# Kernel tuning notes

Hardware: AMD Instinct MI355X
Metric: run time of the kernel (lower is better)

## Reference

```python
import jax, jax.numpy as jnp
import numpy as np

NEG_SLOPE = 0.2
LN_EPS = 1e-5


def _gat_layer(x, src, dst, W, a_src, a_dst, N):
    # x: [N, Fin], W: [Fin, H*C], a_src/a_dst: [H, C]
    H, C = a_src.shape
    h = (x @ W).reshape(N, H, C)
    al_src = (h * a_src).sum(-1)  # [N, H]
    al_dst = (h * a_dst).sum(-1)  # [N, H]
    e = jax.nn.leaky_relu(al_src[src] + al_dst[dst], NEG_SLOPE)  # [E, H]
    m = jax.ops.segment_max(e, dst, num_segments=N)
    e = jnp.exp(e - m[dst])
    denom = jax.ops.segment_sum(e, dst, num_segments=N)
    alpha = e / denom[dst]  # softmax over incoming edges per dst node
    msg = h[src] * alpha[:, :, None]  # [E, H, C]
    return jax.ops.segment_sum(msg, dst, num_segments=N)  # [N, H, C]


def _layer_norm(x, g, b):
    mu = x.mean(-1, keepdims=True)
    var = ((x - mu) ** 2).mean(-1, keepdims=True)
    return (x - mu) * jax.lax.rsqrt(var + LN_EPS) * g + b


def setup_inputs() -> dict:
    key = jax.random.key(0)
    ks = jax.random.split(key, 20)
    N, E, Fin, Ch, H = 50000, 800000, 128, 64, 4
    s = lambda k, shp, sc=0.05: jax.random.normal(k, shp, dtype=jnp.float32) * sc
    return {
        "x": jax.random.normal(ks[0], (N, Fin), dtype=jnp.float32),
        "edge_index": jax.random.randint(ks[1], (2, E), 0, N, dtype=jnp.int64),
        "W1": s(ks[2], (Fin, H * Ch)),
        "att_src1": s(ks[3], (H, Ch)),
        "att_dst1": s(ks[4], (H, Ch)),
        "b1": jnp.zeros((H * Ch,), jnp.float32),
        "ln1_g": jnp.ones((H * Ch,), jnp.float32),
        "ln1_b": jnp.zeros((H * Ch,), jnp.float32),
        "W2": s(ks[5], (H * Ch, Ch)),
        "att_src2": s(ks[6], (1, Ch)),
        "att_dst2": s(ks[7], (1, Ch)),
        "b2": jnp.zeros((Ch,), jnp.float32),
        "ln2_g": jnp.ones((Ch,), jnp.float32),
        "ln2_b": jnp.zeros((Ch,), jnp.float32),
        "fc1_W": s(ks[8], (Ch, Ch // 2)),
        "fc1_b": jnp.zeros((Ch // 2,), jnp.float32),
        "fc2_W": s(ks[9], (Ch // 2, 1)),
        "fc2_b": jnp.zeros((1,), jnp.float32),
    }


def reference(x, edge_index, W1, att_src1, att_dst1, b1, ln1_g, ln1_b,
              W2, att_src2, att_dst2, b2, ln2_g, ln2_b,
              fc1_W, fc1_b, fc2_W, fc2_b):
    N = x.shape[0]
    # PyG GATConv adds self-loops by default
    loop = jnp.arange(N, dtype=edge_index.dtype)
    src = jnp.concatenate([edge_index[0], loop])
    dst = jnp.concatenate([edge_index[1], loop])

    # GAT layer 1 (heads=4, concat) + LayerNorm + ReLU (dropout is identity in eval)
    h = _gat_layer(x, src, dst, W1, att_src1, att_dst1, N).reshape(N, -1) + b1
    h = jax.nn.relu(_layer_norm(h, ln1_g, ln1_b))

    # GAT layer 2 (heads=1) + LayerNorm + ReLU
    h = _gat_layer(h, src, dst, W2, att_src2, att_dst2, N).reshape(N, -1) + b2
    h = jax.nn.relu(_layer_norm(h, ln2_g, ln2_b))

    # MLP head
    h = jax.nn.relu(h @ fc1_W + fc1_b)
    return h @ fc2_W + fc2_b  # [N, 1]
```

## Files before the change

kernel.cpp:

```cpp
#include <hip/hip_runtime.h>
#include <hip/hip_fp16.h>
#include <math.h>

#define NEG_SLOPE 0.2f
#define LN_EPS 1e-5f
#define SCCHUNK 8192
#define PADCAP 64
#define CURPAD 32

typedef __attribute__((ext_vector_type(8))) _Float16 half8;
typedef __attribute__((ext_vector_type(4))) _Float16 half4;
typedef __attribute__((ext_vector_type(4))) float floatx4;

static __device__ __forceinline__ float lrelu(float e) {
    return e > 0.0f ? e : NEG_SLOPE * e;
}

__global__ __launch_bounds__(256) void k_g1sc(
    const float* __restrict__ x, const float* __restrict__ W1,
    const float* __restrict__ as1, const float* __restrict__ ad1,
    _Float16* __restrict__ h1, float* __restrict__ als, float* __restrict__ ald,
    const int* __restrict__ ei, unsigned* __restrict__ cursor,
    unsigned short* __restrict__ eidx,
    int N, int E, int nsc)
{
    const int tid = threadIdx.x;

    if ((int)blockIdx.x < nsc) {
        const unsigned basev = cursor[(size_t)N * CURPAD];
        const int Et = E + N;
        const int i0 = blockIdx.x * SCCHUNK;
#pragma unroll 4
        for (int j = 0; j < SCCHUNK / 256; ++j) {
            int i = i0 + j * 256 + tid;
            if (i < Et) {
                int s, d;
                if (i < E) { s = ei[i]; d = ei[E + i]; } else { s = d = i - E; }
                unsigned pos = atomicAdd(&cursor[(size_t)d * CURPAD], 1u) - basev;
                if (pos < PADCAP) eidx[(size_t)d * PADCAP + pos] = (unsigned short)s;
            }
        }
        return;
    }

    const int tile = blockIdx.x - nsc;
    const int lane = tid & 63, w = tid >> 6;
    const int l15 = lane & 15, quad = lane >> 4;
    const int r_base = tile * 64;

    half8 B[4][4];
    float asv[4], adv[4];
#pragma unroll
    for (int nt = 0; nt < 4; ++nt) {
        const int n = w * 64 + nt * 16 + l15;
        asv[nt] = as1[n]; adv[nt] = ad1[n];
#pragma unroll
        for (int ks = 0; ks < 4; ++ks) {
            const int k0 = ks * 32 + quad * 8;
            half8 b;
#pragma unroll
            for (int j = 0; j < 8; ++j) b[j] = (_Float16)W1[(size_t)(k0 + j) * 256 + n];
            B[ks][nt] = b;
        }
    }

#pragma unroll
    for (int rt = 0; rt < 4; ++rt) {
        const int r0 = r_base + rt * 16;
        int m = r0 + l15; if (m >= N) m = N - 1;
        half8 A[4];
#pragma unroll
        for (int ks = 0; ks < 4; ++ks) {
            const int k0 = ks * 32 + quad * 8;
            const float4* xp = (const float4*)(x + (size_t)m * 128 + k0);
            float4 v0 = xp[0], v1 = xp[1];
            half8 a;
            a[0] = (_Float16)v0.x; a[1] = (_Float16)v0.y; a[2] = (_Float16)v0.z; a[3] = (_Float16)v0.w;
            a[4] = (_Float16)v1.x; a[5] = (_Float16)v1.y; a[6] = (_Float16)v1.z; a[7] = (_Float16)v1.w;
            A[ks] = a;
        }
        floatx4 C[4];
#pragma unroll
        for (int nt = 0; nt < 4; ++nt) C[nt] = (floatx4){0.f, 0.f, 0.f, 0.f};
#pragma unroll
        for (int ks = 0; ks < 4; ++ks)
#pragma unroll
            for (int nt = 0; nt < 4; ++nt)
                C[nt] = __builtin_amdgcn_mfma_f32_16x16x32_f16(A[ks], B[ks][nt], C[nt], 0, 0, 0);

#pragma unroll
        for (int reg = 0; reg < 4; ++reg) {
            const int row = r0 + quad * 4 + reg;
            float vs = 0.f, vd = 0.f;
#pragma unroll
            for (int nt = 0; nt < 4; ++nt) {
                float c = C[nt][reg];
                if (row < N) h1[(size_t)row * 256 + w * 64 + nt * 16 + l15] = (_Float16)c;
                vs += c * asv[nt]; vd += c * adv[nt];
            }
#pragma unroll
            for (int o = 1; o < 16; o <<= 1) { vs += __shfl_xor(vs, o); vd += __shfl_xor(vd, o); }
            if (l15 == 0 && row < N) { als[row * 4 + w] = vs; ald[row * 4 + w] = vd; }
        }
    }
}

__global__ __launch_bounds__(256) void k_agg1(
    const _Float16* __restrict__ h1, const float* __restrict__ als, const float* __restrict__ ald,
    const unsigned* __restrict__ cursor, const unsigned short* __restrict__ eidx,
    const float* __restrict__ b1, const float* __restrict__ g1, const float* __restrict__ be1,
    _Float16* __restrict__ hln1, int N)
{
    __shared__ float alp[4][64][4];
    __shared__ int   srcl[4][64];
    const int wv = threadIdx.x >> 6, lane = threadIdx.x & 63;
    int n = blockIdx.x * 4 + wv;
    if (n >= N) n = N - 1;
    const int base = n * PADCAP;
    const unsigned basev = cursor[(size_t)N * CURPAD];
    int deg = (int)(cursor[(size_t)n * CURPAD] - basev); if (deg > PADCAP) deg = PADCAP;
    const float4 ad = ((const float4*)ald)[n];

    const int srcv = eidx[base + (lane < deg ? lane : deg - 1)];
    float e0 = -1e30f, e1 = -1e30f, e2 = -1e30f, e3 = -1e30f;
    if (lane < deg) {
        float4 a4 = ((const float4*)als)[srcv];
        e0 = lrelu(a4.x + ad.x);
        e1 = lrelu(a4.y + ad.y);
        e2 = lrelu(a4.z + ad.z);
        e3 = lrelu(a4.w + ad.w);
    }
    float m0 = e0, m1 = e1, m2 = e2, m3 = e3;
#pragma unroll
    for (int o = 32; o; o >>= 1) {
        m0 = fmaxf(m0, __shfl_xor(m0, o));
        m1 = fmaxf(m1, __shfl_xor(m1, o));
        m2 = fmaxf(m2, __shfl_xor(m2, o));
        m3 = fmaxf(m3, __shfl_xor(m3, o));
    }
    float p0 = __expf(e0 - m0), p1 = __expf(e1 - m1);
    float p2 = __expf(e2 - m2), p3 = __expf(e3 - m3);
    float s0 = p0, s1 = p1, s2 = p2, s3 = p3;
#pragma unroll
    for (int o = 32; o; o >>= 1) {
        s0 += __shfl_xor(s0, o);
        s1 += __shfl_xor(s1, o);
        s2 += __shfl_xor(s2, o);
        s3 += __shfl_xor(s3, o);
    }
    float4 av;
    av.x = p0 / s0; av.y = p1 / s1; av.z = p2 / s2; av.w = p3 / s3;
    *(float4*)(&alp[wv][lane][0]) = av;
    srcl[wv][lane] = srcv;

    const int half_ = lane >> 5, l31 = lane & 31, hd = l31 >> 3;
    float4 a0 = make_float4(0.f, 0.f, 0.f, 0.f);
    float4 a1 = make_float4(0.f, 0.f, 0.f, 0.f);
    const int degr = (deg + 7) & ~7;
    for (int eb = 0; eb < degr; eb += 8) {
#pragma unroll
        for (int u = 0; u < 4; ++u) {
            const int e = eb + 2 * u + half_;
            int s = srcl[wv][e];
            float ae = alp[wv][e][hd];
            half8 v = *(const half8*)(h1 + (size_t)s * 256 + l31 * 8);
            a0.x = fmaf((float)v[0], ae, a0.x);
            a0.y = fmaf((float)v[1], ae, a0.y);
            a0.z = fmaf((float)v[2], ae, a0.z);
            a0.w = fmaf((float)v[3], ae, a0.w);
            a1.x = fmaf((float)v[4], ae, a1.x);
            a1.y = fmaf((float)v[5], ae, a1.y);
            a1.z = fmaf((float)v[6], ae, a1.z);
            a1.w = fmaf((float)v[7], ae, a1.w);
        }
    }
    a0.x += __shfl_xor(a0.x, 32); a0.y += __shfl_xor(a0.y, 32);
    a0.z += __shfl_xor(a0.z, 32); a0.w += __shfl_xor(a0.w, 32);
    a1.x += __shfl_xor(a1.x, 32); a1.y += __shfl_xor(a1.y, 32);
    a1.z += __shfl_xor(a1.z, 32); a1.w += __shfl_xor(a1.w, 32);

    const float4 bb0 = ((const float4*)b1)[l31 * 2];
    const float4 bb1 = ((const float4*)b1)[l31 * 2 + 1];
    float y0 = a0.x + bb0.x, y1 = a0.y + bb0.y, y2 = a0.z + bb0.z, y3 = a0.w + bb0.w;
    float y4 = a1.x + bb1.x, y5 = a1.y + bb1.y, y6 = a1.z + bb1.z, y7 = a1.w + bb1.w;
    float ps  = y0 + y1 + y2 + y3 + y4 + y5 + y6 + y7;
    float pss = y0*y0 + y1*y1 + y2*y2 + y3*y3 + y4*y4 + y5*y5 + y6*y6 + y7*y7;
#pragma unroll
    for (int o = 32; o; o >>= 1) { ps += __shfl_xor(ps, o); pss += __shfl_xor(pss, o); }
    float mu = ps * (1.f / 512.f);
    float var = pss * (1.f / 512.f) - mu * mu;
    float rstd = rsqrtf(var + LN_EPS);
    const float4 gg0 = ((const float4*)g1)[l31 * 2];
    const float4 gg1 = ((const float4*)g1)[l31 * 2 + 1];
    const float4 be0 = ((const float4*)be1)[l31 * 2];
    const float4 be1v = ((const float4*)be1)[l31 * 2 + 1];
    if (lane < 32) {
        half8 outv;
        outv[0] = (_Float16)fmaxf((y0 - mu) * rstd * gg0.x + be0.x, 0.f);
        outv[1] = (_Float16)fmaxf((y1 - mu) * rstd * gg0.y + be0.y, 0.f);
        outv[2] = (_Float16)fmaxf((y2 - mu) * rstd * gg0.z + be0.z, 0.f);
        outv[3] = (_Float16)fmaxf((y3 - mu) * rstd * gg0.w + be0.w, 0.f);
        outv[4] = (_Float16)fmaxf((y4 - mu) * rstd * gg1.x + be1v.x, 0.f);
        outv[5] = (_Float16)fmaxf((y5 - mu) * rstd * gg1.y + be1v.y, 0.f);
        outv[6] = (_Float16)fmaxf((y6 - mu) * rstd * gg1.z + be1v.z, 0.f);
        outv[7] = (_Float16)fmaxf((y7 - mu) * rstd * gg1.w + be1v.w, 0.f);
        *(half8*)(hln1 + (size_t)n * 256 + l31 * 8) = outv;
    }
}

__global__ __launch_bounds__(256) void k_gemm2(
    const _Float16* __restrict__ hln1, const float* __restrict__ W2,
    const float* __restrict__ as2, const float* __restrict__ ad2,
    _Float16* __restrict__ h2, float* __restrict__ als2, float* __restrict__ ald2, int N)
{
    __shared__ float ps_s[4][64], ps_d[4][64];
    const int lane = threadIdx.x & 63, w = threadIdx.x >> 6;
    const int l15 = lane & 15, quad = lane >> 4;
    const int r_base = blockIdx.x * 64;

    const int n = w * 16 + l15;
    const float asv = as2[n], adv = ad2[n];
    half8 B[8];
#pragma unroll
    for (int ks = 0; ks < 8; ++ks) {
        const int k0 = ks * 32 + quad * 8;
        half8 b;
#pragma unroll
        for (int j = 0; j < 8; ++j) b[j] = (_Float16)W2[(size_t)(k0 + j) * 64 + n];
        B[ks] = b;
    }

#pragma unroll
    for (int rt = 0; rt < 4; ++rt) {
        const int r0 = r_base + rt * 16;
        int m = r0 + l15; if (m >= N) m = N - 1;
        floatx4 C = (floatx4){0.f, 0.f, 0.f, 0.f};
#pragma unroll
        for (int ks = 0; ks < 8; ++ks) {
            half8 a = *(const half8*)(hln1 + (size_t)m * 256 + ks * 32 + quad * 8);
            C = __builtin_amdgcn_mfma_f32_16x16x32_f16(a, B[ks], C, 0, 0, 0);
        }
#pragma unroll
        for (int reg = 0; reg < 4; ++reg) {
            const int row = r0 + quad * 4 + reg;
            float c = C[reg];
            if (row < N) h2[(size_t)row * 64 + n] = (_Float16)c;
            float vs = c * asv, vd = c * adv;
#pragma unroll
            for (int o = 1; o < 16; o <<= 1) { vs += __shfl_xor(vs, o); vd += __shfl_xor(vd, o); }
            if (l15 == 0) {
                ps_s[w][rt * 16 + quad * 4 + reg] = vs;
                ps_d[w][rt * 16 + quad * 4 + reg] = vd;
            }
        }
    }
    __syncthreads();
    const int t = threadIdx.x;
    if (t < 64) {
        const int row = r_base + t;
        if (row < N) {
            als2[row] = ps_s[0][t] + ps_s[1][t] + ps_s[2][t] + ps_s[3][t];
            ald2[row] = ps_d[0][t] + ps_d[1][t] + ps_d[2][t] + ps_d[3][t];
        }
    }
}

__global__ __launch_bounds__(256) void k_agg2(
    const _Float16* __restrict__ h2, const float* __restrict__ als, const float* __restrict__ ald,
    const unsigned* __restrict__ cursor, const unsigned short* __restrict__ eidx,
    const float* __restrict__ b2, const float* __restrict__ g2, const float* __restrict__ be2,
    const float* __restrict__ fc1W, const float* __restrict__ fc1b,
    const float* __restrict__ fc2W, const float* __restrict__ fc2b,
    float* __restrict__ out, int N)
{
    __shared__ float sh[4][64];
    __shared__ float alp2[4][64];
    __shared__ int   src2[4][64];
    const int wv = threadIdx.x >> 6, lane = threadIdx.x & 63;
    int n = blockIdx.x * 4 + wv;
    if (n >= N) n = N - 1;
    const int base = n * PADCAP;
    const unsigned basev = cursor[(size_t)N * CURPAD];
    int deg = (int)(cursor[(size_t)n * CURPAD] - basev); if (deg > PADCAP) deg = PADCAP;
    const float adn = ald[n];

    const int srcv = eidx[base + (lane < deg ? lane : deg - 1)];
    float e = -1e30f;
    if (lane < deg) e = lrelu(als[srcv] + adn);
    float m = e;
#pragma unroll
    for (int o = 32; o; o >>= 1) m = fmaxf(m, __shfl_xor(m, o));
    float p = __expf(e - m);
    float s = p;
#pragma unroll
    for (int o = 32; o; o >>= 1) s += __shfl_xor(s, o);
    alp2[wv][lane] = p / s;
    src2[wv][lane] = srcv;

    const int grp = lane >> 4, l15 = lane & 15;
    float4 acc = make_float4(0.f, 0.f, 0.f, 0.f);
    const int degr = (deg + 7) & ~7;
    for (int eb = 0; eb < degr; eb += 8) {
#pragma unroll
        for (int u = 0; u < 2; ++u) {
            const int e2 = eb + 4 * u + grp;
            int sidx = src2[wv][e2];
            float a_e = alp2[wv][e2];
            half4 v = *(const half4*)(h2 + (size_t)sidx * 64 + l15 * 4);
            acc.x = fmaf((float)v.x, a_e, acc.x);
            acc.y = fmaf((float)v.y, a_e, acc.y);
            acc.z = fmaf((float)v.z, a_e, acc.z);
            acc.w = fmaf((float)v.w, a_e, acc.w);
        }
    }
    acc.x += __shfl_xor(acc.x, 16); acc.y += __shfl_xor(acc.y, 16);
    acc.z += __shfl_xor(acc.z, 16); acc.w += __shfl_xor(acc.w, 16);
    acc.x += __shfl_xor(acc.x, 32); acc.y += __shfl_xor(acc.y, 32);
    acc.z += __shfl_xor(acc.z, 32); acc.w += __shfl_xor(acc.w, 32);

    const float4 bb = ((const float4*)b2)[l15];
    float y0 = acc.x + bb.x, y1 = acc.y + bb.y, y2 = acc.z + bb.z, y3 = acc.w + bb.w;
    float ps = y0 + y1 + y2 + y3;
    float pss = y0*y0 + y1*y1 + y2*y2 + y3*y3;
#pragma unroll
    for (int o = 32; o; o >>= 1) { ps += __shfl_xor(ps, o); pss += __shfl_xor(pss, o); }
    float mu = ps * (1.f / 256.f);
    float var = pss * (1.f / 256.f) - mu * mu;
    float rstd = rsqrtf(var + LN_EPS);
    const float4 gg = ((const float4*)g2)[l15];
    const float4 bev = ((const float4*)be2)[l15];
    if (grp == 0) {
        float4 r;
        r.x = fmaxf((y0 - mu) * rstd * gg.x + bev.x, 0.f);
        r.y = fmaxf((y1 - mu) * rstd * gg.y + bev.y, 0.f);
        r.z = fmaxf((y2 - mu) * rstd * gg.z + bev.z, 0.f);
        r.w = fmaxf((y3 - mu) * rstd * gg.w + bev.w, 0.f);
        *(float4*)(&sh[wv][l15 * 4]) = r;
    }

    if (lane < 32) {
        float a1 = fc1b[lane];
#pragma unroll 8
        for (int k = 0; k < 64; ++k) a1 += sh[wv][k] * fc1W[k * 32 + lane];
        a1 = fmaxf(a1, 0.f);
        float t = a1 * fc2W[lane];
#pragma unroll
        for (int o = 16; o; o >>= 1) t += __shfl_xor(t, o);
        if (lane == 0) out[n] = t + fc2b[0];
    }
}

extern "C" void kernel_launch(void* const* d_in, const int* in_sizes, int n_in,
                              void* d_out, int out_size, void* d_ws, size_t ws_size,
                              hipStream_t stream)
{
    const float* x   = (const float*)d_in[0];
    const int* ei    = (const int*)d_in[1];
    const float* W1  = (const float*)d_in[2];
    const float* as1 = (const float*)d_in[3];
    const float* ad1 = (const float*)d_in[4];
    const float* b1  = (const float*)d_in[5];
    const float* g1  = (const float*)d_in[6];
    const float* be1 = (const float*)d_in[7];
    const float* W2  = (const float*)d_in[8];
    const float* as2 = (const float*)d_in[9];
    const float* ad2 = (const float*)d_in[10];
    const float* b2  = (const float*)d_in[11];
    const float* g2  = (const float*)d_in[12];
    const float* be2 = (const float*)d_in[13];
    const float* fc1W = (const float*)d_in[14];
    const float* fc1b = (const float*)d_in[15];
    const float* fc2W = (const float*)d_in[16];
    const float* fc2b = (const float*)d_in[17];
    float* out = (float*)d_out;

    const int N = in_sizes[0] / 128;
    const int E = in_sizes[1] / 2;
    const int Et = E + N;
    const int nsc = (Et + SCCHUNK - 1) / SCCHUNK;
    const int ntiles = (N + 63) / 64;

    char* p = (char*)d_ws;
    auto carve = [&](size_t bytes) {
        void* q = p;
        p += (bytes + 255) & ~(size_t)255;
        return q;
    };
    _Float16* h1    = (_Float16*)carve((size_t)N * 256 * 2);
    _Float16* hln1h = (_Float16*)carve((size_t)N * 256 * 2);
    _Float16* h2    = (_Float16*)carve((size_t)N * 64 * 2);
    float* als1 = (float*)carve((size_t)N * 4 * 4);
    float* ald1 = (float*)carve((size_t)N * 4 * 4);
    float* als2 = (float*)carve((size_t)N * 4);
    float* ald2 = (float*)carve((size_t)N * 4);
    unsigned* cursor = (unsigned*)carve((size_t)(N + 1) * CURPAD * 4);
    unsigned short* eidx = (unsigned short*)carve((size_t)N * PADCAP * 2);

    k_g1sc<<<nsc + ntiles, 256, 0, stream>>>(x, W1, as1, ad1, h1, als1, ald1,
                                             ei, cursor, eidx, N, E, nsc);
    k_agg1<<<(N + 3) / 4, 256, 0, stream>>>(h1, als1, ald1, cursor, eidx, b1, g1, be1, hln1h, N);
    k_gemm2<<<(N + 63) / 64, 256, 0, stream>>>(hln1h, W2, as2, ad2, h2, als2, ald2, N);
    k_agg2<<<(N + 3) / 4, 256, 0, stream>>>(h2, als2, ald2, cursor, eidx,
                                            b2, g2, be2, fc1W, fc1b, fc2W, fc2b, out, N);
}
```

Baseline: 285.7 us.

## Fuse layer-1 aggregation with layer-2 GEMM via shared-memory staging

```diff
diff --git a/kernel.cpp b/kernel.cpp
--- a/kernel.cpp
+++ b/kernel.cpp
@@ -105,159 +105,149 @@
     }
 }
 
-__global__ __launch_bounds__(256) void k_agg1(
+__global__ __launch_bounds__(1024) void k_agg1g2(
     const _Float16* __restrict__ h1, const float* __restrict__ als, const float* __restrict__ ald,
     const unsigned* __restrict__ cursor, const unsigned short* __restrict__ eidx,
     const float* __restrict__ b1, const float* __restrict__ g1, const float* __restrict__ be1,
-    _Float16* __restrict__ hln1, int N)
-{
-    __shared__ float alp[4][64][4];
-    __shared__ int   srcl[4][64];
-    const int wv = threadIdx.x >> 6, lane = threadIdx.x & 63;
-    int n = blockIdx.x * 4 + wv;
-    if (n >= N) n = N - 1;
-    const int base = n * PADCAP;
-    const unsigned basev = cursor[(size_t)N * CURPAD];
-    int deg = (int)(cursor[(size_t)n * CURPAD] - basev); if (deg > PADCAP) deg = PADCAP;
-    const float4 ad = ((const float4*)ald)[n];
-
-    const int srcv = eidx[base + (lane < deg ? lane : deg - 1)];
-    float e0 = -1e30f, e1 = -1e30f, e2 = -1e30f, e3 = -1e30f;
-    if (lane < deg) {
-        float4 a4 = ((const float4*)als)[srcv];
-        e0 = lrelu(a4.x + ad.x);
-        e1 = lrelu(a4.y + ad.y);
-        e2 = lrelu(a4.z + ad.z);
-        e3 = lrelu(a4.w + ad.w);
-    }
-    float m0 = e0, m1 = e1, m2 = e2, m3 = e3;
-#pragma unroll
-    for (int o = 32; o; o >>= 1) {
-        m0 = fmaxf(m0, __shfl_xor(m0, o));
-        m1 = fmaxf(m1, __shfl_xor(m1, o));
-        m2 = fmaxf(m2, __shfl_xor(m2, o));
-        m3 = fmaxf(m3, __shfl_xor(m3, o));
-    }
-    float p0 = __expf(e0 - m0), p1 = __expf(e1 - m1);
-    float p2 = __expf(e2 - m2), p3 = __expf(e3 - m3);
-    float s0 = p0, s1 = p1, s2 = p2, s3 = p3;
-#pragma unroll
-    for (int o = 32; o; o >>= 1) {
-        s0 += __shfl_xor(s0, o);
-        s1 += __shfl_xor(s1, o);
-        s2 += __shfl_xor(s2, o);
-        s3 += __shfl_xor(s3, o);
-    }
-    float4 av;
-    av.x = p0 / s0; av.y = p1 / s1; av.z = p2 / s2; av.w = p3 / s3;
-    *(float4*)(&alp[wv][lane][0]) = av;
-    srcl[wv][lane] = srcv;
-
-    const int half_ = lane >> 5, l31 = lane & 31, hd = l31 >> 3;
-    float4 a0 = make_float4(0.f, 0.f, 0.f, 0.f);
-    float4 a1 = make_float4(0.f, 0.f, 0.f, 0.f);
-    const int degr = (deg + 7) & ~7;
-    for (int eb = 0; eb < degr; eb += 8) {
-#pragma unroll
-        for (int u = 0; u < 4; ++u) {
-            const int e = eb + 2 * u + half_;
-            int s = srcl[wv][e];
-            float ae = alp[wv][e][hd];
-            half8 v = *(const half8*)(h1 + (size_t)s * 256 + l31 * 8);
-            a0.x = fmaf((float)v[0], ae, a0.x);
-            a0.y = fmaf((float)v[1], ae, a0.y);
-            a0.z = fmaf((float)v[2], ae, a0.z);
-            a0.w = fmaf((float)v[3], ae, a0.w);
-            a1.x = fmaf((float)v[4], ae, a1.x);
-            a1.y = fmaf((float)v[5], ae, a1.y);
-            a1.z = fmaf((float)v[6], ae, a1.z);
-            a1.w = fmaf((float)v[7], ae, a1.w);
-        }
-    }
-    a0.x += __shfl_xor(a0.x, 32); a0.y += __shfl_xor(a0.y, 32);
-    a0.z += __shfl_xor(a0.z, 32); a0.w += __shfl_xor(a0.w, 32);
-    a1.x += __shfl_xor(a1.x, 32); a1.y += __shfl_xor(a1.y, 32);
-    a1.z += __shfl_xor(a1.z, 32); a1.w += __shfl_xor(a1.w, 32);
-
-    const float4 bb0 = ((const float4*)b1)[l31 * 2];
-    const float4 bb1 = ((const float4*)b1)[l31 * 2 + 1];
-    float y0 = a0.x + bb0.x, y1 = a0.y + bb0.y, y2 = a0.z + bb0.z, y3 = a0.w + bb0.w;
-    float y4 = a1.x + bb1.x, y5 = a1.y + bb1.y, y6 = a1.z + bb1.z, y7 = a1.w + bb1.w;
-    float ps  = y0 + y1 + y2 + y3 + y4 + y5 + y6 + y7;
-    float pss = y0*y0 + y1*y1 + y2*y2 + y3*y3 + y4*y4 + y5*y5 + y6*y6 + y7*y7;
-#pragma unroll
-    for (int o = 32; o; o >>= 1) { ps += __shfl_xor(ps, o); pss += __shfl_xor(pss, o); }
-    float mu = ps * (1.f / 512.f);
-    float var = pss * (1.f / 512.f) - mu * mu;
-    float rstd = rsqrtf(var + LN_EPS);
-    const float4 gg0 = ((const float4*)g1)[l31 * 2];
-    const float4 gg1 = ((const float4*)g1)[l31 * 2 + 1];
-    const float4 be0 = ((const float4*)be1)[l31 * 2];
-    const float4 be1v = ((const float4*)be1)[l31 * 2 + 1];
-    if (lane < 32) {
-        half8 outv;
-        outv[0] = (_Float16)fmaxf((y0 - mu) * rstd * gg0.x + be0.x, 0.f);
-        outv[1] = (_Float16)fmaxf((y1 - mu) * rstd * gg0.y + be0.y, 0.f);
-        outv[2] = (_Float16)fmaxf((y2 - mu) * rstd * gg0.z + be0.z, 0.f);
-        outv[3] = (_Float16)fmaxf((y3 - mu) * rstd * gg0.w + be0.w, 0.f);
-        outv[4] = (_Float16)fmaxf((y4 - mu) * rstd * gg1.x + be1v.x, 0.f);
-        outv[5] = (_Float16)fmaxf((y5 - mu) * rstd * gg1.y + be1v.y, 0.f);
-        outv[6] = (_Float16)fmaxf((y6 - mu) * rstd * gg1.z + be1v.z, 0.f);
-        outv[7] = (_Float16)fmaxf((y7 - mu) * rstd * gg1.w + be1v.w, 0.f);
-        *(half8*)(hln1 + (size_t)n * 256 + l31 * 8) = outv;
-    }
-}
-
-__global__ __launch_bounds__(256) void k_gemm2(
-    const _Float16* __restrict__ hln1, const float* __restrict__ W2,
-    const float* __restrict__ as2, const float* __restrict__ ad2,
+    const float* __restrict__ W2, const float* __restrict__ as2, const float* __restrict__ ad2,
     _Float16* __restrict__ h2, float* __restrict__ als2, float* __restrict__ ald2, int N)
 {
+    __shared__ float alp[16][64][4];
+    __shared__ int   srcl[16][64];
+    __shared__ _Float16 hln[64][264];
     __shared__ float ps_s[4][64], ps_d[4][64];
-    const int lane = threadIdx.x & 63, w = threadIdx.x >> 6;
+
+    const int wv = threadIdx.x >> 6, lane = threadIdx.x & 63;
+    const int nb = blockIdx.x * 64;
+    const unsigned basev = cursor[(size_t)N * CURPAD];
+    const int half_ = lane >> 5, l31 = lane & 31, hd8 = l31 >> 3;
+
+#pragma unroll 1
+    for (int nl = 0; nl < 4; ++nl) {
+        const int rloc = wv * 4 + nl;
+        int n = nb + rloc;
+        if (n >= N) n = N - 1;
+        const int base = n * PADCAP;
+        int deg = (int)(cursor[(size_t)n * CURPAD] - basev); if (deg > PADCAP) deg = PADCAP;
+        const float4 ad = ((const float4*)ald)[n];
+
+        const int srcv = eidx[base + (lane < deg ? lane : deg - 1)];
+        float e0 = -1e30f, e1 = -1e30f, e2 = -1e30f, e3 = -1e30f;
+        if (lane < deg) {
+            float4 a4 = ((const float4*)als)[srcv];
+            e0 = lrelu(a4.x + ad.x);
+            e1 = lrelu(a4.y + ad.y);
+            e2 = lrelu(a4.z + ad.z);
+            e3 = lrelu(a4.w + ad.w);
+        }
+        float m0 = e0, m1 = e1, m2 = e2, m3 = e3;
+#pragma unroll
+        for (int o = 32; o; o >>= 1) {
+            m0 = fmaxf(m0, __shfl_xor(m0, o));
+            m1 = fmaxf(m1, __shfl_xor(m1, o));
+            m2 = fmaxf(m2, __shfl_xor(m2, o));
+            m3 = fmaxf(m3, __shfl_xor(m3, o));
+        }
+        float p0 = __expf(e0 - m0), p1 = __expf(e1 - m1);
+        float p2 = __expf(e2 - m2), p3 = __expf(e3 - m3);
+        float s0 = p0, s1 = p1, s2 = p2, s3 = p3;
+#pragma unroll
+        for (int o = 32; o; o >>= 1) {
+            s0 += __shfl_xor(s0, o);
+            s1 += __shfl_xor(s1, o);
+            s2 += __shfl_xor(s2, o);
+            s3 += __shfl_xor(s3, o);
+        }
+        float4 av;
+        av.x = p0 / s0; av.y = p1 / s1; av.z = p2 / s2; av.w = p3 / s3;
+        *(float4*)(&alp[wv][lane][0]) = av;
+        srcl[wv][lane] = srcv;
+
+        float4 a0 = make_float4(0.f, 0.f, 0.f, 0.f);
+        float4 a1 = make_float4(0.f, 0.f, 0.f, 0.f);
+        const int degr = (deg + 7) & ~7;
+        for (int eb = 0; eb < degr; eb += 8) {
+#pragma unroll
+            for (int u = 0; u < 4; ++u) {
+                const int e = eb + 2 * u + half_;
+                int s = srcl[wv][e];
+                float ae = alp[wv][e][hd8];
+                half8 v = *(const half8*)(h1 + (size_t)s * 256 + l31 * 8);
+                a0.x = fmaf((float)v[0], ae, a0.x);
+                a0.y = fmaf((float)v[1], ae, a0.y);
+                a0.z = fmaf((float)v[2], ae, a0.z);
+                a0.w = fmaf((float)v[3], ae, a0.w);
+                a1.x = fmaf((float)v[4], ae, a1.x);
+                a1.y = fmaf((float)v[5], ae, a1.y);
+                a1.z = fmaf((float)v[6], ae, a1.z);
+                a1.w = fmaf((float)v[7], ae, a1.w);
+            }
+        }
+        a0.x += __shfl_xor(a0.x, 32); a0.y += __shfl_xor(a0.y, 32);
+        a0.z += __shfl_xor(a0.z, 32); a0.w += __shfl_xor(a0.w, 32);
+        a1.x += __shfl_xor(a1.x, 32); a1.y += __shfl_xor(a1.y, 32);
+        a1.z += __shfl_xor(a1.z, 32); a1.w += __shfl_xor(a1.w, 32);
+
+        const float4 bb0 = ((const float4*)b1)[l31 * 2];
+        const float4 bb1 = ((const float4*)b1)[l31 * 2 + 1];
+        float y0 = a0.x + bb0.x, y1 = a0.y + bb0.y, y2 = a0.z + bb0.z, y3 = a0.w + bb0.w;
+        float y4 = a1.x + bb1.x, y5 = a1.y + bb1.y, y6 = a1.z + bb1.z, y7 = a1.w + bb1.w;
+        float ps  = y0 + y1 + y2 + y3 + y4 + y5 + y6 + y7;
+        float pss = y0*y0 + y1*y1 + y2*y2 + y3*y3 + y4*y4 + y5*y5 + y6*y6 + y7*y7;
+#pragma unroll
+        for (int o = 32; o; o >>= 1) { ps += __shfl_xor(ps, o); pss += __shfl_xor(pss, o); }
+        float mu = ps * (1.f / 512.f);
+        float var = pss * (1.f / 512.f) - mu * mu;
+        float rstd = rsqrtf(var + LN_EPS);
+        const float4 gg0 = ((const float4*)g1)[l31 * 2];
+        const float4 gg1 = ((const float4*)g1)[l31 * 2 + 1];
+        const float4 be0 = ((const float4*)be1)[l31 * 2];
+        const float4 be1v = ((const float4*)be1)[l31 * 2 + 1];
+        if (lane < 32) {
+            half8 outv;
+            outv[0] = (_Float16)fmaxf((y0 - mu) * rstd * gg0.x + be0.x, 0.f);
+            outv[1] = (_Float16)fmaxf((y1 - mu) * rstd * gg0.y + be0.y, 0.f);
+            outv[2] = (_Float16)fmaxf((y2 - mu) * rstd * gg0.z + be0.z, 0.f);
+            outv[3] = (_Float16)fmaxf((y3 - mu) * rstd * gg0.w + be0.w, 0.f);
+            outv[4] = (_Float16)fmaxf((y4 - mu) * rstd * gg1.x + be1v.x, 0.f);
+            outv[5] = (_Float16)fmaxf((y5 - mu) * rstd * gg1.y + be1v.y, 0.f);
+            outv[6] = (_Float16)fmaxf((y6 - mu) * rstd * gg1.z + be1v.z, 0.f);
+            outv[7] = (_Float16)fmaxf((y7 - mu) * rstd * gg1.w + be1v.w, 0.f);
+            *(half8*)(&hln[rloc][l31 * 8]) = outv;
+        }
+    }
+
+    __syncthreads();
+
     const int l15 = lane & 15, quad = lane >> 4;
-    const int r_base = blockIdx.x * 64;
-
-    const int n = w * 16 + l15;
-    const float asv = as2[n], adv = ad2[n];
-    half8 B[8];
+    const int rt = wv >> 2, ct = wv & 3;
+    const int nch = ct * 16 + l15;
+    const float asv = as2[nch], adv = ad2[nch];
+    floatx4 C = (floatx4){0.f, 0.f, 0.f, 0.f};
 #pragma unroll
     for (int ks = 0; ks < 8; ++ks) {
         const int k0 = ks * 32 + quad * 8;
+        half8 a = *(const half8*)(&hln[rt * 16 + l15][k0]);
         half8 b;
 #pragma unroll
-        for (int j = 0; j < 8; ++j) b[j] = (_Float16)W2[(size_t)(k0 + j) * 64 + n];
-        B[ks] = b;
-    }
-
-#pragma unroll
-    for (int rt = 0; rt < 4; ++rt) {
-        const int r0 = r_base + rt * 16;
-        int m = r0 + l15; if (m >= N) m = N - 1;
-        floatx4 C = (floatx4){0.f, 0.f, 0.f, 0.f};
-#pragma unroll
-        for (int ks = 0; ks < 8; ++ks) {
-            half8 a = *(const half8*)(hln1 + (size_t)m * 256 + ks * 32 + quad * 8);
-            C = __builtin_amdgcn_mfma_f32_16x16x32_f16(a, B[ks], C, 0, 0, 0);
-        }
-#pragma unroll
-        for (int reg = 0; reg < 4; ++reg) {
-            const int row = r0 + quad * 4 + reg;
-            float c = C[reg];
-            if (row < N) h2[(size_t)row * 64 + n] = (_Float16)c;
-            float vs = c * asv, vd = c * adv;
-#pragma unroll
-            for (int o = 1; o < 16; o <<= 1) { vs += __shfl_xor(vs, o); vd += __shfl_xor(vd, o); }
-            if (l15 == 0) {
-                ps_s[w][rt * 16 + quad * 4 + reg] = vs;
-                ps_d[w][rt * 16 + quad * 4 + reg] = vd;
-            }
-        }
+        for (int j = 0; j < 8; ++j) b[j] = (_Float16)W2[(size_t)(k0 + j) * 64 + nch];
+        C = __builtin_amdgcn_mfma_f32_16x16x32_f16(a, b, C, 0, 0, 0);
+    }
+#pragma unroll
+    for (int reg = 0; reg < 4; ++reg) {
+        const int m = rt * 16 + quad * 4 + reg;
+        const int row = nb + m;
+        float c = C[reg];
+        if (row < N) h2[(size_t)row * 64 + nch] = (_Float16)c;
+        float vs = c * asv, vd = c * adv;
+#pragma unroll
+        for (int o = 1; o < 16; o <<= 1) { vs += __shfl_xor(vs, o); vd += __shfl_xor(vd, o); }
+        if (l15 == 0) { ps_s[ct][m] = vs; ps_d[ct][m] = vd; }
     }
     __syncthreads();
     const int t = threadIdx.x;
     if (t < 64) {
-        const int row = r_base + t;
+        const int row = nb + t;
         if (row < N) {
             als2[row] = ps_s[0][t] + ps_s[1][t] + ps_s[2][t] + ps_s[3][t];
             ald2[row] = ps_d[0][t] + ps_d[1][t] + ps_d[2][t] + ps_d[3][t];
@@ -387,7 +377,6 @@
         return q;
     };
     _Float16* h1    = (_Float16*)carve((size_t)N * 256 * 2);
-    _Float16* hln1h = (_Float16*)carve((size_t)N * 256 * 2);
     _Float16* h2    = (_Float16*)carve((size_t)N * 64 * 2);
     float* als1 = (float*)carve((size_t)N * 4 * 4);
     float* ald1 = (float*)carve((size_t)N * 4 * 4);
@@ -398,8 +387,9 @@
 
     k_g1sc<<<nsc + ntiles, 256, 0, stream>>>(x, W1, as1, ad1, h1, als1, ald1,
                                              ei, cursor, eidx, N, E, nsc);
-    k_agg1<<<(N + 3) / 4, 256, 0, stream>>>(h1, als1, ald1, cursor, eidx, b1, g1, be1, hln1h, N);
-    k_gemm2<<<(N + 63) / 64, 256, 0, stream>>>(hln1h, W2, as2, ad2, h2, als2, ald2, N);
+    k_agg1g2<<<(N + 63) / 64, 1024, 0, stream>>>(h1, als1, ald1, cursor, eidx,
+                                                 b1, g1, be1, W2, as2, ad2,
+                                                 h2, als2, ald2, N);
     k_agg2<<<(N + 3) / 4, 256, 0, stream>>>(h2, als2, ald2, cursor, eidx,
                                             b2, g2, be2, fc1W, fc1b, fc2W, fc2b, out, N);
 }
```

Measured after the change: 305.5 us. 1.07x slower.
